# Kernel optimization log

Measured on AMD Instinct MI355X. Metric: run time of the kernel, lower is better.

The kernel has to match this reference:

```python
import jax, jax.numpy as jnp
import numpy as np

T, B, OBS, H, M1, M2, A = 64, 2048, 48, 256, 512, 256, 12
LOG2PI = float(np.log(2.0 * np.pi))
LOG_STD_MIN, LOG_STD_MAX = -5.0, 2.0
LN_EPS = 1e-5


def _elu(x):
    return jnp.where(x > 0, x, jnp.expm1(x))


def setup_inputs() -> dict:
    key = jax.random.key(0)
    ks = jax.random.split(key, 10)
    s = lambda k, shape, sc=0.05: jax.random.normal(k, shape, jnp.float32) * sc
    return dict(
        x=jax.random.normal(ks[0], (T, B, OBS), jnp.float32),
        done=jax.random.randint(ks[1], (T, B), 0, 2).astype(jnp.int32),
        h0=jnp.zeros((B, H), jnp.float32),
        c0=jnp.zeros((B, H), jnp.float32),
        W_ih=s(ks[2], (4 * H, OBS)),
        W_hh=s(ks[3], (4 * H, H)),
        b_ih=jnp.zeros((4 * H,), jnp.float32),
        b_hh=jnp.zeros((4 * H,), jnp.float32),
        ln_g=jnp.ones((H,), jnp.float32),
        ln_b=jnp.zeros((H,), jnp.float32),
        W1=s(ks[4], (H, M1)),
        b1=jnp.zeros((M1,), jnp.float32),
        W2=s(ks[5], (M1, M2)),
        b2=jnp.zeros((M2,), jnp.float32),
        Wm=s(ks[6], (M2, A), 0.01),
        bm=jnp.zeros((A,), jnp.float32),
        Ws=s(ks[7], (M2, A), 0.01),
        bs=jnp.zeros((A,), jnp.float32),
    )


def reference(x, h0, c0, W_ih, W_hh, b_ih, b_hh, ln_g, ln_b,
              W1, b1, W2, b2, Wm, bm, Ws, bs, done):
    # Precompute input-side gate projections for all timesteps: [T, B, 4H]
    xg = jnp.einsum('tbi,gi->tbg', x, W_ih) + b_ih + b_hh
    keep = 1.0 - done.astype(jnp.float32)  # [T, B]; reset state where done==1

    def step(carry, inp):
        h, c = carry
        xgt, m = inp
        h = h * m[:, None]
        c = c * m[:, None]
        g = xgt + h @ W_hh.T  # [B, 4H], PyTorch gate order i,f,g,o
        i, f, gg, o = jnp.split(g, 4, axis=-1)
        c = jax.nn.sigmoid(f) * c + jax.nn.sigmoid(i) * jnp.tanh(gg)
        h = jax.nn.sigmoid(o) * jnp.tanh(c)
        return (h, c), h

    (_, _), hs = jax.lax.scan(step, (h0, c0), (xg, keep))
    hflat = hs.reshape(T * B, H)

    # LayerNorm
    mu = hflat.mean(-1, keepdims=True)
    var = ((hflat - mu) ** 2).mean(-1, keepdims=True)
    y = (hflat - mu) / jnp.sqrt(var + LN_EPS) * ln_g + ln_b

    # Actor MLP (ELU after every Linear, per build_mlp)
    y = _elu(y @ W1 + b1)
    y = _elu(y @ W2 + b2)

    mean = y @ Wm + bm
    logstd = jnp.clip(y @ Ws + bs, LOG_STD_MIN, LOG_STD_MAX)
    # deterministic action == mean, so (a - mu)^2 / (2 sigma^2) == 0
    logp = (-logstd - 0.5 * LOG2PI).sum(-1)
    ent = (0.5 + 0.5 * LOG2PI + logstd).sum(-1)
    # [T*B, A+2]: action mean, log_prob, entropy
    return jnp.concatenate([mean, logp[:, None], ent[:, None]], axis=-1)
```

## Files before the change

### kernel.cpp

```cpp
#include <hip/hip_runtime.h>
#include <hip/hip_bf16.h>
#include <math.h>

#define T_   64
#define B_   2048
#define OBS_ 48
#define H_   256
#define M1_  512
#define M2_  256
#define A_   12
#define BH_  (B_ * H_)
#define KP_  320
#define GROUPS_  128
#define SLICES_  2
#define RPB_     16

typedef unsigned short u16;
typedef unsigned long long u64;
typedef __attribute__((ext_vector_type(8))) short bf16x8;
typedef __attribute__((ext_vector_type(4))) float f32x4;

static __device__ __forceinline__ u16 f2b(float f) {
    __hip_bfloat16 h = __float2bfloat16(f);
    return *reinterpret_cast<u16*>(&h);
}
static __device__ __forceinline__ float b2f(u16 u) {
    union { unsigned u32v; float f; } v; v.u32v = ((unsigned)u) << 16; return v.f;
}
static __device__ __forceinline__ float sigm(float x) {
    return 1.0f / (1.0f + __expf(-x));
}
static __device__ __forceinline__ float tanh_fast(float x) {
    x = fminf(fmaxf(x, -15.0f), 15.0f);
    float e = __expf(2.0f * x);
    return (e - 1.0f) / (e + 1.0f);
}
static __device__ __forceinline__ float elu(float x) {
    return x > 0.0f ? x : (__expf(x) - 1.0f);
}

__global__ void prep_xpad(const float* __restrict__ x, u16* __restrict__ xpad,
                          unsigned* __restrict__ cnt) {
    if (blockIdx.x == 0 && threadIdx.x < GROUPS_ * SLICES_) cnt[threadIdx.x] = 0;
    const int gid = blockIdx.x * 256 + threadIdx.x;
    const int r = gid >> 3, k0 = (gid & 7) * 8;
    u16 tmp[8];
    if (k0 < OBS_) {
        const float4 f0 = *(const float4*)(x + (size_t)r * OBS_ + k0);
        const float4 f1 = *(const float4*)(x + (size_t)r * OBS_ + k0 + 4);
        tmp[0] = f2b(f0.x); tmp[1] = f2b(f0.y); tmp[2] = f2b(f0.z); tmp[3] = f2b(f0.w);
        tmp[4] = f2b(f1.x); tmp[5] = f2b(f1.y); tmp[6] = f2b(f1.z); tmp[7] = f2b(f1.w);
    } else {
        #pragma unroll
        for (int i = 0; i < 8; ++i) tmp[i] = 0;
    }
    *(uint4*)(xpad + (size_t)gid * 8) = *(uint4*)tmp;
}

__global__ void prep_weights(const float* __restrict__ W_ih, const float* __restrict__ W_hh,
                             const float* __restrict__ W1,  const float* __restrict__ W2,
                             const float* __restrict__ Wm,  const float* __restrict__ Ws,
                             u16* __restrict__ Wcat, u16* __restrict__ W1T,
                             u16* __restrict__ W2T,  u16* __restrict__ WhT) {
    const int b = blockIdx.x, tid = threadIdx.x;
    if (b < 1024) {
        const int s = b >> 9, w = (b >> 6) & 7, g = (b >> 4) & 3, jj = b & 15;
        const int src = g * 256 + s * 128 + w * 16 + jj;
        for (int k = tid; k < KP_; k += 256) {
            float v;
            if (k < OBS_)     v = W_ih[src * OBS_ + k];
            else if (k < 64)  v = 0.0f;
            else if (k < 192) v = W_hh[src * H_ + s * 128 + (k - 64)];
            else              v = W_hh[src * H_ + (1 - s) * 128 + (k - 192)];
            Wcat[b * KP_ + k] = f2b(v);
        }
    } else if (b < 1536) {
        const int n = b - 1024;
        W1T[n * 256 + tid] = f2b(W1[tid * M1_ + n]);
    } else if (b < 1792) {
        const int n = b - 1536;
        W2T[n * 512 + tid]       = f2b(W2[tid * M2_ + n]);
        W2T[n * 512 + tid + 256] = f2b(W2[(tid + 256) * M2_ + n]);
    } else {
        const int n = b - 1792;
        float v = 0.0f;
        if (n < 12)                 v = Wm[tid * A_ + n];
        else if (n >= 16 && n < 28) v = Ws[tid * A_ + (n - 16)];
        WhT[n * 256 + tid] = f2b(v);
    }
}

#define ASM_(row, chunk) (a_sm + (size_t)(row) * 320 + (size_t)(((chunk) ^ ((row) & 7)) << 3))

__global__ __launch_bounds__(512, 2) void lstm_sync2(
    const u16*  __restrict__ xpad,
    const int*  __restrict__ done,
    const float* __restrict__ h0,
    const float* __restrict__ c0,
    u16*        __restrict__ hs,
    const u16*  __restrict__ Wcat,
    const float* __restrict__ b_ih,
    const float* __restrict__ b_hh,
    unsigned*   __restrict__ cnt)
{
    __shared__ u16 a_sm[RPB_ * 320];
    __shared__ unsigned okf;

    const int tid  = threadIdx.x;
    const int lane = tid & 63;
    const int w    = tid >> 6;
    const int quad = lane >> 4, l16 = lane & 15;
    const int grp  = blockIdx.x >> 1;
    const int s    = blockIdx.x & 1;
    const int b0   = grp * RPB_;
    const int j    = s * 128 + w * 16 + l16;
    const int jrel = w * 16 + l16;
    const int pc0  = (1 - s) * 128;

    float bsum[4];
    #pragma unroll
    for (int g = 0; g < 4; ++g) bsum[g] = b_ih[g * 256 + j] + b_hh[g * 256 + j];

    float cst[4];
    #pragma unroll
    for (int r = 0; r < 4; ++r) {
        const int row = b0 + quad * 4 + r;
        cst[r] = done[row] ? 0.0f : c0[(size_t)row * H_ + j];
    }

    bf16x8 Bs[4][10];
    #pragma unroll
    for (int g = 0; g < 4; ++g) {
        const u16* wp = Wcat + (size_t)(((s * 8 + w) * 4 + g) * 16 + l16) * KP_ + quad * 8;
        #pragma unroll
        for (int kt = 0; kt < 10; ++kt)
            Bs[g][kt] = *(const bf16x8*)(wp + kt * 32);
    }

    if ((tid & 3) == 0) {
        const int idx = tid >> 2, row = idx >> 3, seg = idx & 7;
        *(uint4*)ASM_(row, seg) =
            *(const uint4*)(xpad + (size_t)(b0 + row) * 64 + seg * 8);
    }
    {
        const int row = tid >> 5, c8 = tid & 31;
        const int cglob = c8 * 8;
        const int dn = done[b0 + row];
        const float* hr = h0 + (size_t)(b0 + row) * H_ + cglob;
        u16 tmp[8];
        #pragma unroll
        for (int e = 0; e < 8; ++e) tmp[e] = dn ? (u16)0 : f2b(hr[e]);
        const int chunk = (((cglob >> 7) == s) ? 8 : 24) + ((cglob & 127) >> 3);
        *(uint4*)ASM_(row, chunk) = *(uint4*)tmp;
    }
    __syncthreads();

    for (int t = 0; t < T_; ++t) {
        unsigned fv = 0;
        if (tid == 0 && t > 0)
            fv = __hip_atomic_load(&cnt[blockIdx.x ^ 1], __ATOMIC_RELAXED,
                                   __HIP_MEMORY_SCOPE_AGENT);

        f32x4 acc[4];
        #pragma unroll
        for (int g = 0; g < 4; ++g) acc[g] = (f32x4){0, 0, 0, 0};
        #pragma unroll
        for (int kt = 0; kt < 6; ++kt) {
            const bf16x8 af = *(const bf16x8*)ASM_(l16, kt * 4 + quad);
            #pragma unroll
            for (int g = 0; g < 4; ++g)
                acc[g] = __builtin_amdgcn_mfma_f32_16x16x32_bf16(af, Bs[g][kt], acc[g], 0, 0, 0);
        }

        if (tid == 0) okf = (t == 0 || fv >= (unsigned)t) ? 1u : 0u;
        __syncthreads();
        {
            int guard = 0;
            while (!okf) {
                if (tid == 0) {
                    __builtin_amdgcn_s_sleep(1);
                    fv = __hip_atomic_load(&cnt[blockIdx.x ^ 1], __ATOMIC_RELAXED,
                                           __HIP_MEMORY_SCOPE_AGENT);
                    if (fv >= (unsigned)t || ++guard > (1 << 22)) okf = 1u;
                }
                __syncthreads();
            }
        }

        if (t > 0 && tid < 256) {
            const u16* hst = hs + (size_t)t * BH_;
            const int row = tid >> 4, q = tid & 15;
            const int dn = done[(size_t)t * B_ + b0 + row];
            uint4 hv = *(const uint4*)(hst + (size_t)(b0 + row) * H_ + pc0 + q * 8);
            if (dn) hv = make_uint4(0u, 0u, 0u, 0u);
            *(uint4*)ASM_(row, 24 + q) = hv;
        }
        if (t + 1 < T_ && tid >= 256 && tid < 384) {
            const int idx = tid - 256, row = idx >> 3, seg = idx & 7;
            *(uint4*)ASM_(row, seg) =
                *(const uint4*)(xpad + ((size_t)(t + 1) * B_ + b0 + row) * 64 + seg * 8);
        }
        __syncthreads();

        #pragma unroll
        for (int kt = 6; kt < 10; ++kt) {
            const bf16x8 af = *(const bf16x8*)ASM_(l16, kt * 4 + quad);
            #pragma unroll
            for (int g = 0; g < 4; ++g)
                acc[g] = __builtin_amdgcn_mfma_f32_16x16x32_bf16(af, Bs[g][kt], acc[g], 0, 0, 0);
        }

        u16* hs1 = hs + (size_t)(t + 1) * BH_;
        #pragma unroll
        for (int r = 0; r < 4; ++r) {
            const int rowl = quad * 4 + r;
            const int rowg = b0 + rowl;
            const float gi = acc[0][r] + bsum[0];
            const float gf = acc[1][r] + bsum[1];
            const float gg = acc[2][r] + bsum[2];
            const float go = acc[3][r] + bsum[3];
            const float cn = sigm(gf) * cst[r] + sigm(gi) * tanh_fast(gg);
            const float h  = sigm(go) * tanh_fast(cn);
            const float kp = (t + 1 < T_)
                ? (done[(size_t)(t + 1) * B_ + rowg] ? 0.0f : 1.0f) : 1.0f;
            cst[r] = cn * kp;
            const int e = 64 + jrel;
            *(ASM_(rowl, e >> 3) + (e & 7)) = f2b(h * kp);
            const unsigned hb = (unsigned)f2b(h);
            const unsigned ob = (unsigned)__shfl_xor((int)hb, 1);
            if ((l16 & 1) == 0) {
                const unsigned val = hb | (ob << 16);
                __hip_atomic_store((unsigned*)(hs1 + (size_t)rowg * H_ + (j & ~1)), val,
                                   __ATOMIC_RELAXED, __HIP_MEMORY_SCOPE_AGENT);
            }
        }
        __syncthreads();

        if (tid == 0 && t + 1 < T_)
            __hip_atomic_store(&cnt[blockIdx.x], (unsigned)(t + 1),
                               __ATOMIC_RELAXED, __HIP_MEMORY_SCOPE_AGENT);
    }
}

#define SY(row, col) ((size_t)(row) * 256 + ((((col) >> 3) ^ ((row) & 7)) << 3) + ((col) & 7))

__global__ __launch_bounds__(512, 4) void mlp_mfma64(
    const u16*  __restrict__ hs,
    float*      __restrict__ out,
    const float* __restrict__ lng, const float* __restrict__ lnb,
    const u16*  __restrict__ W1T, const float* __restrict__ b1,
    const u16*  __restrict__ W2T, const float* __restrict__ b2,
    const u16*  __restrict__ WhT,
    const float* __restrict__ bm, const float* __restrict__ bs)
{
    __shared__ u16 ybf[64 * 256];
    __shared__ u16 yh [64 * 256];

    const int tid  = threadIdx.x;
    const int lane = tid & 63;
    const int wave = tid >> 6;
    const int quad = lane >> 4, l16 = lane & 15;
    const int row0 = blockIdx.x * 64;

    {
        const float4 gv = *(const float4*)(lng + lane * 4);
        const float4 bv = *(const float4*)(lnb + lane * 4);
        #pragma unroll
        for (int rr = 0; rr < 8; ++rr) {
            const int r = wave * 8 + rr;
            const u64 hv8 = __builtin_nontemporal_load(
                (const u64*)(hs + (size_t)(row0 + r) * H_ + lane * 4));
            const u16 h0v = (u16)(hv8 & 0xffff), h1v = (u16)((hv8 >> 16) & 0xffff);
            const u16 h2v = (u16)((hv8 >> 32) & 0xffff), h3v = (u16)(hv8 >> 48);
            const float v0 = b2f(h0v), v1 = b2f(h1v), v2 = b2f(h2v), v3 = b2f(h3v);
            float s  = v0 + v1 + v2 + v3;
            float ss = v0 * v0 + v1 * v1 + v2 * v2 + v3 * v3;
            #pragma unroll
            for (int off = 32; off > 0; off >>= 1) {
                s  += __shfl_down(s,  off);
                ss += __shfl_down(ss, off);
            }
            s = __shfl(s, 0); ss = __shfl(ss, 0);
            const float mu   = s * (1.0f / 256.0f);
            const float rstd = rsqrtf(ss * (1.0f / 256.0f) - mu * mu + 1e-5f);
            ushort4 o;
            o.x = f2b((v0 - mu) * rstd * gv.x + bv.x);
            o.y = f2b((v1 - mu) * rstd * gv.y + bv.y);
            o.z = f2b((v2 - mu) * rstd * gv.z + bv.z);
            o.w = f2b((v3 - mu) * rstd * gv.w + bv.w);
            *(ushort4*)(ybf + SY(r, lane * 4)) = o;
        }
    }
    __syncthreads();

    f32x4 acc2[4][2];
    #pragma unroll
    for (int m = 0; m < 4; ++m)
        #pragma unroll
        for (int j = 0; j < 2; ++j) acc2[m][j] = (f32x4){0,0,0,0};

    #pragma unroll
    for (int ph = 0; ph < 2; ++ph) {
        {
            f32x4 acc[4][2];
            #pragma unroll
            for (int m = 0; m < 4; ++m)
                #pragma unroll
                for (int j = 0; j < 2; ++j) acc[m][j] = (f32x4){0,0,0,0};
            const int n0 = ph * 256 + wave * 32;
            const u16* wp0 = W1T + (size_t)(n0 + l16) * 256 + quad * 8;
            const u16* wp1 = W1T + (size_t)(n0 + 16 + l16) * 256 + quad * 8;
            #pragma unroll
            for (int kt = 0; kt < 8; ++kt) {
                const int k0 = kt * 32;
                const bf16x8 bw0 = *(const bf16x8*)(wp0 + k0);
                const bf16x8 bw1 = *(const bf16x8*)(wp1 + k0);
                #pragma unroll
                for (int m = 0; m < 4; ++m) {
                    const bf16x8 af = *(const bf16x8*)(ybf + SY(m * 16 + l16, k0 + quad * 8));
                    acc[m][0] = __builtin_amdgcn_mfma_f32_16x16x32_bf16(af, bw0, acc[m][0], 0, 0, 0);
                    acc[m][1] = __builtin_amdgcn_mfma_f32_16x16x32_bf16(af, bw1, acc[m][1], 0, 0, 0);
                }
            }
            const float bb0 = b1[n0 + l16], bb1 = b1[n0 + 16 + l16];
            __syncthreads();
            #pragma unroll
            for (int m = 0; m < 4; ++m)
                #pragma unroll
                for (int r = 0; r < 4; ++r) {
                    const int row = m * 16 + quad * 4 + r;
                    yh[SY(row, wave * 32 + l16)]      = f2b(elu(acc[m][0][r] + bb0));
                    yh[SY(row, wave * 32 + 16 + l16)] = f2b(elu(acc[m][1][r] + bb1));
                }
        }
        __syncthreads();

        {
            const int n0 = wave * 32;
            const u16* wp0 = W2T + (size_t)(n0 + l16) * 512 + ph * 256 + quad * 8;
            const u16* wp1 = W2T + (size_t)(n0 + 16 + l16) * 512 + ph * 256 + quad * 8;
            #pragma unroll
            for (int kt = 0; kt < 8; ++kt) {
                const int k0 = kt * 32;
                const bf16x8 bw0 = *(const bf16x8*)(wp0 + k0);
                const bf16x8 bw1 = *(const bf16x8*)(wp1 + k0);
                #pragma unroll
                for (int m = 0; m < 4; ++m) {
                    const bf16x8 af = *(const bf16x8*)(yh + SY(m * 16 + l16, k0 + quad * 8));
                    acc2[m][0] = __builtin_amdgcn_mfma_f32_16x16x32_bf16(af, bw0, acc2[m][0], 0, 0, 0);
                    acc2[m][1] = __builtin_amdgcn_mfma_f32_16x16x32_bf16(af, bw1, acc2[m][1], 0, 0, 0);
                }
            }
        }
        __syncthreads();
    }

    {
        const float bb0 = b2[wave * 32 + l16], bb1 = b2[wave * 32 + 16 + l16];
        #pragma unroll
        for (int m = 0; m < 4; ++m)
            #pragma unroll
            for (int r = 0; r < 4; ++r) {
                const int row = m * 16 + quad * 4 + r;
                ybf[SY(row, wave * 32 + l16)]      = f2b(elu(acc2[m][0][r] + bb0));
                ybf[SY(row, wave * 32 + 16 + l16)] = f2b(elu(acc2[m][1][r] + bb1));
            }
    }
    __syncthreads();

    float* lsf = (float*)yh;
    if (wave < 4) {
        f32x4 a0 = {0,0,0,0}, a1 = {0,0,0,0};
        const u16* wp0 = WhT + (size_t)l16 * 256 + quad * 8;
        const u16* wp1 = WhT + (size_t)(16 + l16) * 256 + quad * 8;
        #pragma unroll
        for (int kt = 0; kt < 8; ++kt) {
            const int k0 = kt * 32;
            const bf16x8 af  = *(const bf16x8*)(ybf + SY(wave * 16 + l16, k0 + quad * 8));
            const bf16x8 bw0 = *(const bf16x8*)(wp0 + k0);
            const bf16x8 bw1 = *(const bf16x8*)(wp1 + k0);
            a0 = __builtin_amdgcn_mfma_f32_16x16x32_bf16(af, bw0, a0, 0, 0, 0);
            a1 = __builtin_amdgcn_mfma_f32_16x16x32_bf16(af, bw1, a1, 0, 0, 0);
        }
        if (l16 < 12) {
            const float bbm = bm[l16], bbs = bs[l16];
            #pragma unroll
            for (int r = 0; r < 4; ++r) {
                const int row = wave * 16 + quad * 4 + r;
                out[(size_t)(row0 + row) * 14 + l16] = a0[r] + bbm;
                lsf[row * 16 + l16] = fminf(fmaxf(a1[r] + bbs, -5.0f), 2.0f);
            }
        }
    }
    __syncthreads();
    if (tid < 64) {
        float s = 0.0f;
        #pragma unroll
        for (int q = 0; q < 12; ++q) s += lsf[tid * 16 + q];
        const float LOG2PI = 1.8378770664093453f;
        out[(size_t)(row0 + tid) * 14 + 12] = -s - 6.0f * LOG2PI;
        out[(size_t)(row0 + tid) * 14 + 13] =  s + 6.0f + 6.0f * LOG2PI;
    }
}

extern "C" void kernel_launch(void* const* d_in, const int* in_sizes, int n_in,
                              void* d_out, int out_size, void* d_ws, size_t ws_size,
                              hipStream_t stream) {
    (void)in_sizes; (void)n_in; (void)out_size; (void)ws_size;
    const float* x    = (const float*)d_in[0];
    const int*   done = (const int*)  d_in[1];
    const float* h0   = (const float*)d_in[2];
    const float* c0   = (const float*)d_in[3];
    const float* W_ih = (const float*)d_in[4];
    const float* W_hh = (const float*)d_in[5];
    const float* b_ih = (const float*)d_in[6];
    const float* b_hh = (const float*)d_in[7];
    const float* lng  = (const float*)d_in[8];
    const float* lnb  = (const float*)d_in[9];
    const float* W1   = (const float*)d_in[10];
    const float* b1   = (const float*)d_in[11];
    const float* W2   = (const float*)d_in[12];
    const float* b2   = (const float*)d_in[13];
    const float* Wm   = (const float*)d_in[14];
    const float* bm   = (const float*)d_in[15];
    const float* Ws   = (const float*)d_in[16];
    const float* bs   = (const float*)d_in[17];
    float* out = (float*)d_out;

    unsigned char* p = (unsigned char*)d_ws;
    u16* hs    = (u16*)p;              p += (size_t)(T_ + 1) * BH_ * 2;
    u16* xpad  = (u16*)p;              p += (size_t)T_ * B_ * 64 * 2;
    u16* Wcat  = (u16*)p;              p += (size_t)1024 * KP_ * 2;
    u16* W1T   = (u16*)p;              p += (size_t)M1_ * H_ * 2;
    u16* W2T   = (u16*)p;              p += (size_t)M2_ * M1_ * 2;
    u16* WhT   = (u16*)p;              p += (size_t)32 * H_ * 2;
    unsigned* cnt = (unsigned*)p;      p += 1024;

    prep_xpad<<<(T_ * B_ * 8) / 256, 256, 0, stream>>>(x, xpad, cnt);
    prep_weights<<<1824, 256, 0, stream>>>(W_ih, W_hh, W1, W2, Wm, Ws,
                                           Wcat, W1T, W2T, WhT);

    lstm_sync2<<<GROUPS_ * SLICES_, 512, 0, stream>>>(
        xpad, done, h0, c0, hs, Wcat, b_ih, b_hh, cnt);

    mlp_mfma64<<<(T_ * B_) / 64, 512, 0, stream>>>(
        hs + BH_, out, lng, lnb, W1T, b1, W2T, b2, WhT, bm, bs);
}
```

Before: 581.4 us.

## Merge prep kernels, remap LSTM block pairing, split MLP hidden into four phases

The two preprocessing kernels become one launch, removing a kernel launch. The LSTM block-to-slice mapping changes so partner blocks are 128 apart rather than adjacent, which may change CU placement of the communicating pairs. The MLP kernel now processes the 512-wide hidden layer in four 128-column phases, halving the intermediate shared buffer and accumulator registers so launch bounds can target 6 blocks per SM. In exchange it adds more barriers per block and re-reads the activation tile once per phase.

```diff
diff --git a/kernel.cpp b/kernel.cpp
--- a/kernel.cpp
+++ b/kernel.cpp
@@ -39,30 +39,32 @@
     return x > 0.0f ? x : (__expf(x) - 1.0f);
 }
 
-__global__ void prep_xpad(const float* __restrict__ x, u16* __restrict__ xpad,
-                          unsigned* __restrict__ cnt) {
-    if (blockIdx.x == 0 && threadIdx.x < GROUPS_ * SLICES_) cnt[threadIdx.x] = 0;
-    const int gid = blockIdx.x * 256 + threadIdx.x;
-    const int r = gid >> 3, k0 = (gid & 7) * 8;
-    u16 tmp[8];
-    if (k0 < OBS_) {
-        const float4 f0 = *(const float4*)(x + (size_t)r * OBS_ + k0);
-        const float4 f1 = *(const float4*)(x + (size_t)r * OBS_ + k0 + 4);
-        tmp[0] = f2b(f0.x); tmp[1] = f2b(f0.y); tmp[2] = f2b(f0.z); tmp[3] = f2b(f0.w);
-        tmp[4] = f2b(f1.x); tmp[5] = f2b(f1.y); tmp[6] = f2b(f1.z); tmp[7] = f2b(f1.w);
-    } else {
-        #pragma unroll
-        for (int i = 0; i < 8; ++i) tmp[i] = 0;
-    }
-    *(uint4*)(xpad + (size_t)gid * 8) = *(uint4*)tmp;
-}
-
-__global__ void prep_weights(const float* __restrict__ W_ih, const float* __restrict__ W_hh,
-                             const float* __restrict__ W1,  const float* __restrict__ W2,
-                             const float* __restrict__ Wm,  const float* __restrict__ Ws,
-                             u16* __restrict__ Wcat, u16* __restrict__ W1T,
-                             u16* __restrict__ W2T,  u16* __restrict__ WhT) {
-    const int b = blockIdx.x, tid = threadIdx.x;
+__global__ void prep_all(const float* __restrict__ x, u16* __restrict__ xpad,
+                         const float* __restrict__ W_ih, const float* __restrict__ W_hh,
+                         const float* __restrict__ W1,  const float* __restrict__ W2,
+                         const float* __restrict__ Wm,  const float* __restrict__ Ws,
+                         u16* __restrict__ Wcat, u16* __restrict__ W1T,
+                         u16* __restrict__ W2T,  u16* __restrict__ WhT,
+                         unsigned* __restrict__ cnt) {
+    const int blk = blockIdx.x, tid = threadIdx.x;
+    if (blk < 4096) {
+        const int gid = blk * 256 + tid;
+        const int r = gid >> 3, k0 = (gid & 7) * 8;
+        u16 tmp[8];
+        if (k0 < OBS_) {
+            const float4 f0 = *(const float4*)(x + (size_t)r * OBS_ + k0);
+            const float4 f1 = *(const float4*)(x + (size_t)r * OBS_ + k0 + 4);
+            tmp[0] = f2b(f0.x); tmp[1] = f2b(f0.y); tmp[2] = f2b(f0.z); tmp[3] = f2b(f0.w);
+            tmp[4] = f2b(f1.x); tmp[5] = f2b(f1.y); tmp[6] = f2b(f1.z); tmp[7] = f2b(f1.w);
+        } else {
+            #pragma unroll
+            for (int i = 0; i < 8; ++i) tmp[i] = 0;
+        }
+        *(uint4*)(xpad + (size_t)gid * 8) = *(uint4*)tmp;
+        return;
+    }
+    const int b = blk - 4096;
+    if (b == 0 && tid < GROUPS_ * SLICES_) cnt[tid] = 0;
     if (b < 1024) {
         const int s = b >> 9, w = (b >> 6) & 7, g = (b >> 4) & 3, jj = b & 15;
         const int src = g * 256 + s * 128 + w * 16 + jj;
@@ -110,8 +112,9 @@
     const int lane = tid & 63;
     const int w    = tid >> 6;
     const int quad = lane >> 4, l16 = lane & 15;
-    const int grp  = blockIdx.x >> 1;
-    const int s    = blockIdx.x & 1;
+    const int grp  = blockIdx.x & 127;
+    const int s    = blockIdx.x >> 7;
+    const int pidx = blockIdx.x ^ 128;
     const int b0   = grp * RPB_;
     const int j    = s * 128 + w * 16 + l16;
     const int jrel = w * 16 + l16;
@@ -158,7 +161,7 @@
     for (int t = 0; t < T_; ++t) {
         unsigned fv = 0;
         if (tid == 0 && t > 0)
-            fv = __hip_atomic_load(&cnt[blockIdx.x ^ 1], __ATOMIC_RELAXED,
+            fv = __hip_atomic_load(&cnt[pidx], __ATOMIC_RELAXED,
                                    __HIP_MEMORY_SCOPE_AGENT);
 
         f32x4 acc[4];
@@ -179,7 +182,7 @@
             while (!okf) {
                 if (tid == 0) {
                     __builtin_amdgcn_s_sleep(1);
-                    fv = __hip_atomic_load(&cnt[blockIdx.x ^ 1], __ATOMIC_RELAXED,
+                    fv = __hip_atomic_load(&cnt[pidx], __ATOMIC_RELAXED,
                                            __HIP_MEMORY_SCOPE_AGENT);
                     if (fv >= (unsigned)t || ++guard > (1 << 22)) okf = 1u;
                 }
@@ -242,9 +245,10 @@
     }
 }
 
-#define SY(row, col) ((size_t)(row) * 256 + ((((col) >> 3) ^ ((row) & 7)) << 3) + ((col) & 7))
-
-__global__ __launch_bounds__(512, 4) void mlp_mfma64(
+#define SY(row, col)  ((size_t)(row) * 256 + ((((col) >> 3) ^ ((row) & 7)) << 3) + ((col) & 7))
+#define SYH(row, col) ((size_t)(row) * 128 + ((((col) >> 3) ^ ((row) & 7)) << 3) + ((col) & 7))
+
+__global__ __launch_bounds__(512, 6) void mlp_mfma64p4(
     const u16*  __restrict__ hs,
     float*      __restrict__ out,
     const float* __restrict__ lng, const float* __restrict__ lnb,
@@ -254,7 +258,7 @@
     const float* __restrict__ bm, const float* __restrict__ bs)
 {
     __shared__ u16 ybf[64 * 256];
-    __shared__ u16 yh [64 * 256];
+    __shared__ u16 yh [64 * 128];
 
     const int tid  = threadIdx.x;
     const int lane = tid & 63;
@@ -300,60 +304,46 @@
         for (int j = 0; j < 2; ++j) acc2[m][j] = (f32x4){0,0,0,0};
 
     #pragma unroll
-    for (int ph = 0; ph < 2; ++ph) {
-        {
-            f32x4 acc[4][2];
-            #pragma unroll
-            for (int m = 0; m < 4; ++m)
-                #pragma unroll
-                for (int j = 0; j < 2; ++j) acc[m][j] = (f32x4){0,0,0,0};
-            const int n0 = ph * 256 + wave * 32;
-            const u16* wp0 = W1T + (size_t)(n0 + l16) * 256 + quad * 8;
-            const u16* wp1 = W1T + (size_t)(n0 + 16 + l16) * 256 + quad * 8;
-            #pragma unroll
-            for (int kt = 0; kt < 8; ++kt) {
-                const int k0 = kt * 32;
-                const bf16x8 bw0 = *(const bf16x8*)(wp0 + k0);
-                const bf16x8 bw1 = *(const bf16x8*)(wp1 + k0);
-                #pragma unroll
-                for (int m = 0; m < 4; ++m) {
-                    const bf16x8 af = *(const bf16x8*)(ybf + SY(m * 16 + l16, k0 + quad * 8));
-                    acc[m][0] = __builtin_amdgcn_mfma_f32_16x16x32_bf16(af, bw0, acc[m][0], 0, 0, 0);
-                    acc[m][1] = __builtin_amdgcn_mfma_f32_16x16x32_bf16(af, bw1, acc[m][1], 0, 0, 0);
-                }
-            }
-            const float bb0 = b1[n0 + l16], bb1 = b1[n0 + 16 + l16];
-            __syncthreads();
-            #pragma unroll
-            for (int m = 0; m < 4; ++m)
-                #pragma unroll
-                for (int r = 0; r < 4; ++r) {
-                    const int row = m * 16 + quad * 4 + r;
-                    yh[SY(row, wave * 32 + l16)]      = f2b(elu(acc[m][0][r] + bb0));
-                    yh[SY(row, wave * 32 + 16 + l16)] = f2b(elu(acc[m][1][r] + bb1));
-                }
-        }
+    for (int p = 0; p < 4; ++p) {
+        f32x4 acc[4];
+        #pragma unroll
+        for (int m = 0; m < 4; ++m) acc[m] = (f32x4){0,0,0,0};
+        const int n1 = p * 128 + wave * 16 + l16;
+        const u16* wp = W1T + (size_t)n1 * 256 + quad * 8;
+        #pragma unroll
+        for (int kt = 0; kt < 8; ++kt) {
+            const bf16x8 bw = *(const bf16x8*)(wp + kt * 32);
+            #pragma unroll
+            for (int m = 0; m < 4; ++m) {
+                const bf16x8 af = *(const bf16x8*)(ybf + SY(m * 16 + l16, kt * 32 + quad * 8));
+                acc[m] = __builtin_amdgcn_mfma_f32_16x16x32_bf16(af, bw, acc[m], 0, 0, 0);
+            }
+        }
+        const float bb = b1[n1];
         __syncthreads();
-
-        {
-            const int n0 = wave * 32;
-            const u16* wp0 = W2T + (size_t)(n0 + l16) * 512 + ph * 256 + quad * 8;
-            const u16* wp1 = W2T + (size_t)(n0 + 16 + l16) * 512 + ph * 256 + quad * 8;
-            #pragma unroll
-            for (int kt = 0; kt < 8; ++kt) {
-                const int k0 = kt * 32;
-                const bf16x8 bw0 = *(const bf16x8*)(wp0 + k0);
-                const bf16x8 bw1 = *(const bf16x8*)(wp1 + k0);
-                #pragma unroll
-                for (int m = 0; m < 4; ++m) {
-                    const bf16x8 af = *(const bf16x8*)(yh + SY(m * 16 + l16, k0 + quad * 8));
-                    acc2[m][0] = __builtin_amdgcn_mfma_f32_16x16x32_bf16(af, bw0, acc2[m][0], 0, 0, 0);
-                    acc2[m][1] = __builtin_amdgcn_mfma_f32_16x16x32_bf16(af, bw1, acc2[m][1], 0, 0, 0);
-                }
-            }
-        }
+        #pragma unroll
+        for (int m = 0; m < 4; ++m)
+            #pragma unroll
+            for (int r = 0; r < 4; ++r)
+                yh[SYH(m * 16 + quad * 4 + r, wave * 16 + l16)] = f2b(elu(acc[m][r] + bb));
         __syncthreads();
-    }
+
+        const int n0 = wave * 32;
+        const u16* wp0 = W2T + (size_t)(n0 + l16) * 512 + p * 128 + quad * 8;
+        const u16* wp1 = W2T + (size_t)(n0 + 16 + l16) * 512 + p * 128 + quad * 8;
+        #pragma unroll
+        for (int kt = 0; kt < 4; ++kt) {
+            const bf16x8 bw0 = *(const bf16x8*)(wp0 + kt * 32);
+            const bf16x8 bw1 = *(const bf16x8*)(wp1 + kt * 32);
+            #pragma unroll
+            for (int m = 0; m < 4; ++m) {
+                const bf16x8 af = *(const bf16x8*)(yh + SYH(m * 16 + l16, kt * 32 + quad * 8));
+                acc2[m][0] = __builtin_amdgcn_mfma_f32_16x16x32_bf16(af, bw0, acc2[m][0], 0, 0, 0);
+                acc2[m][1] = __builtin_amdgcn_mfma_f32_16x16x32_bf16(af, bw1, acc2[m][1], 0, 0, 0);
+            }
+        }
+    }
+    __syncthreads();
 
     {
         const float bb0 = b2[wave * 32 + l16], bb1 = b2[wave * 32 + 16 + l16];
@@ -436,13 +426,12 @@
     u16* WhT   = (u16*)p;              p += (size_t)32 * H_ * 2;
     unsigned* cnt = (unsigned*)p;      p += 1024;
 
-    prep_xpad<<<(T_ * B_ * 8) / 256, 256, 0, stream>>>(x, xpad, cnt);
-    prep_weights<<<1824, 256, 0, stream>>>(W_ih, W_hh, W1, W2, Wm, Ws,
-                                           Wcat, W1T, W2T, WhT);
+    prep_all<<<4096 + 1824, 256, 0, stream>>>(x, xpad, W_ih, W_hh, W1, W2, Wm, Ws,
+                                              Wcat, W1T, W2T, WhT, cnt);
 
     lstm_sync2<<<GROUPS_ * SLICES_, 512, 0, stream>>>(
         xpad, done, h0, c0, hs, Wcat, b_ih, b_hh, cnt);
 
-    mlp_mfma64<<<(T_ * B_) / 64, 512, 0, stream>>>(
+    mlp_mfma64p4<<<(T_ * B_) / 64, 512, 0, stream>>>(
         hs + BH_, out, lng, lnb, W1T, b1, W2T, b2, WhT, bm, bs);
 }
```

Result: slower. 611.9 us (+5.3%).
